# Kernel optimization log

Hardware: AMD Instinct MI355X
Metric: run time of the kernel (lower is better)

The kernel has to match this reference:

```python
import jax, jax.numpy as jnp
import numpy as np

N, E, IN, H, D = 50000, 800000, 256, 4, 32
NEG_SLOPE = 0.2


def setup_inputs() -> dict:
    key = jax.random.key(0)
    ks = jax.random.split(key, 11)
    feat = jax.random.normal(ks[0], (N, IN), jnp.float32)
    src = jax.random.randint(ks[1], (E,), 0, N, jnp.int32)
    dst = jax.random.randint(ks[2], (E,), 0, N, jnp.int32)
    # ppmi in [1, 10) so log(log(ppmi)) path is non-trivial
    ppmi = 1.0 + 9.0 * jax.random.uniform(ks[3], (E,), jnp.float32)
    eps_src = jax.random.normal(ks[4], (N, H, 1), jnp.float32)
    eps_dst = jax.random.normal(ks[5], (N, H, 1), jnp.float32)
    W = jax.random.normal(ks[6], (IN, H * D), jnp.float32) * (1.0 / np.sqrt(IN))
    mu_src = jax.random.normal(ks[7], (1, H, D), jnp.float32) * 0.02
    mu_dst = jax.random.normal(ks[8], (1, H, D), jnp.float32) * 0.02
    lam_src = jax.random.normal(ks[9], (1, H, D), jnp.float32) * 0.02
    lam_dst = jax.random.normal(ks[10], (1, H, D), jnp.float32) * 0.02
    return dict(feat=feat, src=src, dst=dst, ppmi=ppmi, eps_src=eps_src,
                eps_dst=eps_dst, W=W, mu_src=mu_src, mu_dst=mu_dst,
                lam_src=lam_src, lam_dst=lam_dst)


def reference(feat, src, dst, ppmi, eps_src, eps_dst, W, mu_src, mu_dst, lam_src, lam_dst):
    n = feat.shape[0]
    h, d = mu_src.shape[1], mu_src.shape[2]
    ft = (feat @ W).reshape(n, h, d)                      # [N,H,D]
    # per-node attention scalars (src == dst node set here)
    mu_s = (ft * mu_src).sum(-1, keepdims=True)           # [N,H,1]
    lam_s = (ft * lam_src).sum(-1, keepdims=True)
    mu_d = (ft * mu_dst).sum(-1, keepdims=True)
    lam_d = (ft * lam_src).sum(-1, keepdims=True)         # original uses lam_src here (replicated)
    # reparameterize z = eps * exp(0.5*logvar) + mu
    z_src = eps_src * jnp.exp(0.5 * lam_s) + mu_s
    z_dst = eps_dst * jnp.exp(0.5 * lam_d) + mu_d
    e = jax.nn.leaky_relu(z_src[src] + z_dst[dst], NEG_SLOPE)   # [E,H,1]
    scale = jnp.clip(jnp.log(jnp.clip(jnp.log(ppmi), 1.0, None)), 1.0, None)
    e2 = e * scale[:, None, None]
    # edge softmax over destination segments
    emax = jax.ops.segment_max(e2, dst, num_segments=n)   # [N,H,1]
    ee = jnp.exp(e2 - emax[dst])
    denom = jax.ops.segment_sum(ee, dst, num_segments=n)
    a = ee / denom[dst]                                    # [E,H,1]
    # weighted scatter-sum aggregation: u_mul_e + sum
    rst = jax.ops.segment_sum(ft[src] * a, dst, num_segments=n)  # [N,H,D]
    return rst, mu_s + mu_d, lam_s + lam_d
```

## Files before the change

### kernel.cpp

```cpp
#include <hip/hip_runtime.h>

#define N_NODES 50000
#define N_EDGES 800000
#define IN_DIM  256
#define NH      4
#define HD      128
#define NEG_SLOPE 0.2f
#define SCAN_BLOCKS ((N_NODES + 255) / 256)
#define HIST_BLOCKS ((N_EDGES + 255) / 256)
#define WT_BLOCKS   ((HD * IN_DIM) / 256)
#define K1B_BLOCKS  ((N_NODES * NH + 255) / 256)

typedef short          v8s __attribute__((ext_vector_type(8)));
typedef float          v4f __attribute__((ext_vector_type(4)));
typedef float          v2f __attribute__((ext_vector_type(2)));
typedef unsigned short us8 __attribute__((ext_vector_type(8)));
typedef int            v2i __attribute__((ext_vector_type(2)));

__device__ __forceinline__ unsigned short f2bf(float f)
{
    unsigned int u = __float_as_uint(f);
    u += 0x7fffu + ((u >> 16) & 1u);
    return (unsigned short)(u >> 16);
}
__device__ __forceinline__ float bf2f(unsigned int bits16)
{
    return __uint_as_float(bits16 << 16);
}

__device__ __forceinline__ float edge_scale(float p)
{
    const float lp = fmaxf(__logf(p), 1.0f);
    return fmaxf(__logf(lp), 1.0f);
}

__global__ __launch_bounds__(256) void k_wt_hist(
    const float* __restrict__ W, unsigned short* __restrict__ Wt_bf,
    const int* __restrict__ dst, int* __restrict__ counts,
    int* __restrict__ rank)
{
    const int b = blockIdx.x;
    if (b < HIST_BLOCKS) {
        const int e = b * 256 + threadIdx.x;
        if (e < N_EDGES) rank[e] = atomicAdd(&counts[dst[e]], 1);
    } else {
        const int idx = (b - HIST_BLOCKS) * 256 + threadIdx.x;
        const int n = idx >> 8;
        const int k = idx & 255;
        Wt_bf[n * IN_DIM + k] = f2bf(W[(size_t)k * HD + n]);
    }
}

#define AS 40
#define CS 136

__global__ __launch_bounds__(256) void k1_mfma(
    const float* __restrict__ feat, const unsigned short* __restrict__ Wt_bf,
    unsigned short* __restrict__ ft_bf)
{
    __shared__ ushort smem[17408];
    ushort* A_sh = smem;
    ushort* B_sh = smem + 128 * AS;

    const int t    = threadIdx.x;
    const int lane = t & 63;
    const int wv   = t >> 6;
    const int r0   = blockIdx.x * 128;

    const int arow = t >> 3;
    const int akk  = (t & 7) * 4;
    int rA[4];
#pragma unroll
    for (int p = 0; p < 4; ++p) rA[p] = min(r0 + arow + 32 * p, N_NODES - 1);
    const int bn  = t >> 2;
    const int bk8 = (t & 3) * 8;

    float4 fa[4];
    us8    fb[2];

#define LOADC(kc0)                                                              \
    do {                                                                        \
        _Pragma("unroll")                                                       \
        for (int p = 0; p < 4; ++p)                                             \
            fa[p] = *(const float4*)(feat + (size_t)rA[p] * IN_DIM + (kc0) + akk); \
        _Pragma("unroll")                                                       \
        for (int p = 0; p < 2; ++p)                                             \
            fb[p] = *(const us8*)(Wt_bf + (size_t)(bn + 64 * p) * IN_DIM + (kc0) + bk8); \
    } while (0)

    v4f acc[2][8];
#pragma unroll
    for (int i = 0; i < 2; ++i)
#pragma unroll
        for (int j = 0; j < 8; ++j) acc[i][j] = (v4f)(0.0f);

    const int frow = lane & 15;
    const int fq   = lane >> 4;

    LOADC(0);

    for (int c = 0; c < IN_DIM / 32; ++c) {
        __syncthreads();
#pragma unroll
        for (int p = 0; p < 4; ++p) {
            ushort4 u;
            u.x = f2bf(fa[p].x); u.y = f2bf(fa[p].y);
            u.z = f2bf(fa[p].z); u.w = f2bf(fa[p].w);
            *(ushort4*)(A_sh + (arow + 32 * p) * AS + akk) = u;
        }
#pragma unroll
        for (int p = 0; p < 2; ++p)
            *(us8*)(B_sh + (bn + 64 * p) * AS + bk8) = fb[p];
        __syncthreads();

        if (c + 1 < IN_DIM / 32) LOADC((c + 1) * 32);

        v8s a0 = *(const v8s*)(A_sh + (wv * 32 + frow) * AS + fq * 8);
        v8s a1 = *(const v8s*)(A_sh + (wv * 32 + 16 + frow) * AS + fq * 8);
        v8s bfr[8];
#pragma unroll
        for (int nf = 0; nf < 8; ++nf)
            bfr[nf] = *(const v8s*)(B_sh + (nf * 16 + frow) * AS + fq * 8);
#pragma unroll
        for (int nf = 0; nf < 8; ++nf) {
            acc[0][nf] = __builtin_amdgcn_mfma_f32_16x16x32_bf16(
                a0, bfr[nf], acc[0][nf], 0, 0, 0);
            acc[1][nf] = __builtin_amdgcn_mfma_f32_16x16x32_bf16(
                a1, bfr[nf], acc[1][nf], 0, 0, 0);
        }
    }

    __syncthreads();
    ushort* Cw = smem + wv * (32 * CS);
#pragma unroll
    for (int mf = 0; mf < 2; ++mf)
#pragma unroll
        for (int nf = 0; nf < 8; ++nf)
#pragma unroll
            for (int r = 0; r < 4; ++r)
                Cw[(mf * 16 + fq * 4 + r) * CS + nf * 16 + frow] =
                    f2bf(acc[mf][nf][r]);
    __syncthreads();

#pragma unroll
    for (int p = 0; p < 8; ++p) {
        const int row_l = (lane >> 4) + 4 * p;
        const int colv  = (lane & 15) * 8;
        const us8 val = *(const us8*)(Cw + row_l * CS + colv);
        const int grow = r0 + wv * 32 + row_l;
        if (grow < N_NODES)
            *(us8*)(ft_bf + (size_t)grow * HD + colv) = val;
    }
}

__global__ __launch_bounds__(256) void k_k1b_scanlocal(
    const int* __restrict__ counts, int* __restrict__ local,
    int* __restrict__ bsums,
    const unsigned short* __restrict__ ft_bf,
    const float* __restrict__ mu_src, const float* __restrict__ mu_dst,
    const float* __restrict__ lam_src,
    const float* __restrict__ eps_src, const float* __restrict__ eps_dst,
    float* __restrict__ z_src_ws, float* __restrict__ z_dst_ws,
    float* __restrict__ mu_out, float* __restrict__ lam_out)
{
    __shared__ int sh[256];
    const int b = blockIdx.x;
    const int t = threadIdx.x;

    if (b < SCAN_BLOCKS) {
        const int i = b * 256 + t;
        const int v = (i < N_NODES) ? counts[i] : 0;
        sh[t] = v;
        __syncthreads();
#pragma unroll
        for (int off = 1; off < 256; off <<= 1) {
            int x = (t >= off) ? sh[t - off] : 0;
            __syncthreads();
            sh[t] += x;
            __syncthreads();
        }
        if (i < N_NODES) local[i] = sh[t] - v;
        if (t == 255) bsums[b] = sh[255];
        return;
    }

    const int g = (b - SCAN_BLOCKS) * 256 + t;
    if (g >= N_NODES * NH) return;
    const int row = g >> 2;
    const int h   = g & 3;

    const unsigned short* fr = ft_bf + (size_t)row * HD + h * 32;
    const float* ms = mu_src + h * 32;
    const float* md = mu_dst + h * 32;
    const float* ls = lam_src + h * 32;

    float pm = 0.0f, pd = 0.0f, pl = 0.0f;
#pragma unroll
    for (int v = 0; v < 4; ++v) {
        const us8 u = *(const us8*)(fr + v * 8);
#pragma unroll
        for (int j = 0; j < 8; ++j) {
            const float f = bf2f(u[j]);
            const int   i = v * 8 + j;
            pm = fmaf(f, ms[i], pm);
            pd = fmaf(f, md[i], pd);
            pl = fmaf(f, ls[i], pl);
        }
    }
    const float sdev = expf(0.5f * pl);
    z_src_ws[g] = eps_src[g] * sdev + pm;
    z_dst_ws[g] = eps_dst[g] * sdev + pd;
    mu_out[g]   = pm + pd;
    lam_out[g]  = 2.0f * pl;
}

__global__ __launch_bounds__(256) void k_scan_bsums(
    const int* __restrict__ bsums, int* __restrict__ bscan)
{
    __shared__ int sh[256];
    const int t = threadIdx.x;
    const int v = (t < SCAN_BLOCKS) ? bsums[t] : 0;
    sh[t] = v;
    __syncthreads();
#pragma unroll
    for (int off = 1; off < 256; off <<= 1) {
        int x = (t >= off) ? sh[t - off] : 0;
        __syncthreads();
        sh[t] += x;
        __syncthreads();
    }
    if (t < SCAN_BLOCKS) bscan[t] = sh[t] - v;
}

__global__ __launch_bounds__(256) void k_scan_add(
    const int* __restrict__ local, const int* __restrict__ bscan,
    int* __restrict__ offsets)
{
    const int i = blockIdx.x * 256 + threadIdx.x;
    if (i >= N_NODES) return;
    offsets[i] = local[i] + bscan[blockIdx.x];
}

__global__ __launch_bounds__(256) void k_scatter(
    const int* __restrict__ src, const int* __restrict__ dst,
    const float* __restrict__ ppmi, const int* __restrict__ rank,
    const int* __restrict__ offsets, v2i* __restrict__ rec_sorted)
{
    const int e = blockIdx.x * 256 + threadIdx.x;
    if (e >= N_EDGES) return;
    const int d0 = dst[e];
    const int j  = offsets[d0] + rank[e];
    v2i rec;
    rec.x = src[e];
    rec.y = __float_as_int(edge_scale(ppmi[e]));
    __builtin_nontemporal_store(rec, rec_sorted + j);
}

__device__ __forceinline__ float edge_w1(float zs, float zd, float sc)
{
    float v = zs + zd;
    v = (v >= 0.0f) ? v : NEG_SLOPE * v;
    return __expf(v * sc);
}

__global__ __launch_bounds__(256, 8) void k3_csr(
    const int* __restrict__ offsets, const int* __restrict__ counts,
    const v2i* __restrict__ rec_sorted,
    const float* __restrict__ z_src_ws, const float* __restrict__ z_dst_ws,
    const uint4* __restrict__ ft_u128, v2f* __restrict__ rst2)
{
    const int node = blockIdx.x * 4 + (threadIdx.x >> 6);
    const int lane = threadIdx.x & 63;
    const int es   = lane >> 4;
    const int li   = lane & 15;
    const int h    = li >> 2;
    const int start = offsets[node];
    const int deg   = counts[node];
    const float zd  = z_dst_ws[node * NH + h];

    float acc[8] = {0, 0, 0, 0, 0, 0, 0, 0};
    float wsum = 0.0f;

#define K3_EDGE(EI)                                                            \
    do {                                                                       \
        const int  ei  = (EI);                                                 \
        const int  idx = start + ((ei < deg) ? ei : 0);                        \
        const v2i  r   = __builtin_nontemporal_load(rec_sorted + idx);         \
        const float zs = z_src_ws[r.x * NH + h];                               \
        const uint4 f  = ft_u128[(size_t)r.x * 16 + li];                       \
        float w = edge_w1(zs, zd, __int_as_float(r.y));                        \
        if (ei >= deg) w = 0.0f;                                               \
        acc[0] = fmaf(bf2f(f.x & 0xffffu), w, acc[0]);                         \
        acc[1] = fmaf(bf2f(f.x >> 16),     w, acc[1]);                         \
        acc[2] = fmaf(bf2f(f.y & 0xffffu), w, acc[2]);                         \
        acc[3] = fmaf(bf2f(f.y >> 16),     w, acc[3]);                         \
        acc[4] = fmaf(bf2f(f.z & 0xffffu), w, acc[4]);                         \
        acc[5] = fmaf(bf2f(f.z >> 16),     w, acc[5]);                         \
        acc[6] = fmaf(bf2f(f.w & 0xffffu), w, acc[6]);                         \
        acc[7] = fmaf(bf2f(f.w >> 16),     w, acc[7]);                         \
        wsum += w;                                                             \
    } while (0)

    int i = 0;
    for (; i + 16 <= deg; i += 16) {
        K3_EDGE(i + es);
        K3_EDGE(i + 4 + es);
        K3_EDGE(i + 8 + es);
        K3_EDGE(i + 12 + es);
    }
    if (i < deg) {
        K3_EDGE(i + es);
        K3_EDGE(i + 4 + es);
        K3_EDGE(i + 8 + es);
        K3_EDGE(i + 12 + es);
    }

#pragma unroll
    for (int m = 16; m <= 32; m <<= 1) {
        wsum += __shfl_xor(wsum, m, 64);
#pragma unroll
        for (int j = 0; j < 8; ++j) acc[j] += __shfl_xor(acc[j], m, 64);
    }

    const float inv = (wsum > 0.0f) ? 1.0f / wsum : 0.0f;
    v2f o;
    o.x = acc[es * 2] * inv;
    o.y = acc[es * 2 + 1] * inv;
    __builtin_nontemporal_store(o, &rst2[(size_t)node * 64 + li * 4 + es]);
}

extern "C" void kernel_launch(void* const* d_in, const int* in_sizes, int n_in,
                              void* d_out, int out_size, void* d_ws, size_t ws_size,
                              hipStream_t stream)
{
    const float* feat    = (const float*)d_in[0];
    const int*   src     = (const int*)  d_in[1];
    const int*   dst     = (const int*)  d_in[2];
    const float* ppmi    = (const float*)d_in[3];
    const float* eps_src = (const float*)d_in[4];
    const float* eps_dst = (const float*)d_in[5];
    const float* W       = (const float*)d_in[6];
    const float* mu_src  = (const float*)d_in[7];
    const float* mu_dst  = (const float*)d_in[8];
    const float* lam_src = (const float*)d_in[9];

    float* out     = (float*)d_out;
    float* rst     = out;
    float* mu_out  = out + (size_t)N_NODES * HD;
    float* lam_out = mu_out + (size_t)N_NODES * NH;

    char* wsb = (char*)d_ws;
    v2i*            rec_s  = (v2i*)wsb;
    unsigned short* ft_bf  = (unsigned short*)(wsb + (size_t)N_EDGES * 8);
    unsigned short* Wt_bf  = ft_bf + (size_t)N_NODES * HD;
    float*          zs_ws  = (float*)(Wt_bf + (size_t)HD * IN_DIM);
    float*          zd_ws  = zs_ws + (size_t)N_NODES * NH;
    int*            counts = (int*)(zd_ws + (size_t)N_NODES * NH);
    int*            local  = counts + N_NODES;
    int*            offsets= local + N_NODES;
    int*            bsums  = offsets + N_NODES;
    int*            bscan  = bsums + 256;
    int*            rank   = bscan + 256;

    hipMemsetAsync(counts, 0, N_NODES * sizeof(int), stream);

    k_wt_hist<<<HIST_BLOCKS + WT_BLOCKS, 256, 0, stream>>>(
        W, Wt_bf, dst, counts, rank);

    k1_mfma<<<(N_NODES + 127) / 128, 256, 0, stream>>>(feat, Wt_bf, ft_bf);

    k_k1b_scanlocal<<<SCAN_BLOCKS + K1B_BLOCKS, 256, 0, stream>>>(
        counts, local, bsums,
        ft_bf, mu_src, mu_dst, lam_src, eps_src, eps_dst,
        zs_ws, zd_ws, mu_out, lam_out);

    k_scan_bsums<<<1, 256, 0, stream>>>(bsums, bscan);
    k_scan_add<<<SCAN_BLOCKS, 256, 0, stream>>>(local, bscan, offsets);

    k_scatter<<<HIST_BLOCKS, 256, 0, stream>>>(
        src, dst, ppmi, rank, offsets, rec_s);

    k3_csr<<<N_NODES / 4, 256, 0, stream>>>(
        offsets, counts, rec_s, zs_ws, zd_ws,
        (const uint4*)ft_bf, (v2f*)rst);
}
```

Measured before the change: 236.4 us.

## Fuse GEMM epilogue attention scalars and single-pass scan into one kernel

Folds the per-node mu/lam/z computation into the GEMM epilogue, reading the bf16 tile from shared memory instead of reloading ft from global memory. Runs the degree prefix scan as extra blocks of the same launch, with a last-block-done atomic counter doing the block-sum scan. The separate add pass is removed; consumers compute local+bscan on the fly. This cuts three kernel launches and one pass over ft, at the cost of heavier epilogue work and atomic-based cross-block ordering.

```diff
diff --git a/kernel.cpp b/kernel.cpp
--- a/kernel.cpp
+++ b/kernel.cpp
@@ -9,7 +9,7 @@
 #define SCAN_BLOCKS ((N_NODES + 255) / 256)
 #define HIST_BLOCKS ((N_EDGES + 255) / 256)
 #define WT_BLOCKS   ((HD * IN_DIM) / 256)
-#define K1B_BLOCKS  ((N_NODES * NH + 255) / 256)
+#define GEMM_BLOCKS ((N_NODES + 127) / 128)
 
 typedef short          v8s __attribute__((ext_vector_type(8)));
 typedef float          v4f __attribute__((ext_vector_type(4)));
@@ -54,18 +54,70 @@
 #define AS 40
 #define CS 136
 
-__global__ __launch_bounds__(256) void k1_mfma(
+__global__ __launch_bounds__(256) void k_gemm_fused(
     const float* __restrict__ feat, const unsigned short* __restrict__ Wt_bf,
-    unsigned short* __restrict__ ft_bf)
-{
-    __shared__ ushort smem[17408];
+    unsigned short* __restrict__ ft_bf,
+    const int* __restrict__ counts, int* __restrict__ local,
+    int* __restrict__ bsums, int* __restrict__ bscan, int* __restrict__ done,
+    const float* __restrict__ mu_src, const float* __restrict__ mu_dst,
+    const float* __restrict__ lam_src,
+    const float* __restrict__ eps_src, const float* __restrict__ eps_dst,
+    float* __restrict__ z_src_ws, float* __restrict__ z_dst_ws,
+    float* __restrict__ mu_out, float* __restrict__ lam_out)
+{
+    __shared__ ushort smem[17408 + 768];
+    const int t = threadIdx.x;
+    const int b = blockIdx.x;
+
+    if (b >= GEMM_BLOCKS) {
+        int* sh = (int*)smem;
+        __shared__ int lastv;
+        const int sb = b - GEMM_BLOCKS;
+        const int i = sb * 256 + t;
+        const int v = (i < N_NODES) ? counts[i] : 0;
+        sh[t] = v;
+        __syncthreads();
+#pragma unroll
+        for (int off = 1; off < 256; off <<= 1) {
+            int x = (t >= off) ? sh[t - off] : 0;
+            __syncthreads();
+            sh[t] += x;
+            __syncthreads();
+        }
+        if (i < N_NODES) local[i] = sh[t] - v;
+        if (t == 255) atomicExch(&bsums[sb], sh[255]);
+        __syncthreads();
+        if (t == 0) lastv = atomicAdd(done, 1);
+        __syncthreads();
+        if (lastv == SCAN_BLOCKS - 1) {
+            const int v2 = (t < SCAN_BLOCKS) ? atomicAdd(&bsums[t], 0) : 0;
+            sh[t] = v2;
+            __syncthreads();
+#pragma unroll
+            for (int off = 1; off < 256; off <<= 1) {
+                int x = (t >= off) ? sh[t - off] : 0;
+                __syncthreads();
+                sh[t] += x;
+                __syncthreads();
+            }
+            if (t < SCAN_BLOCKS) bscan[t] = sh[t] - v2;
+        }
+        return;
+    }
+
     ushort* A_sh = smem;
     ushort* B_sh = smem + 128 * AS;
-
-    const int t    = threadIdx.x;
+    float*  tab  = (float*)(smem + 17408);
+
+    if (t < 128) {
+        tab[t]       = mu_src[t];
+        tab[128 + t] = mu_dst[t];
+        tab[256 + t] = lam_src[t];
+    }
+
     const int lane = t & 63;
     const int wv   = t >> 6;
-    const int r0   = blockIdx.x * 128;
+    const int r0   = b * 128;
 
     const int arow = t >> 3;
     const int akk  = (t & 7) * 4;
@@ -151,105 +203,48 @@
         if (grow < N_NODES)
             *(us8*)(ft_bf + (size_t)grow * HD + colv) = val;
     }
-}
-
-__global__ __launch_bounds__(256) void k_k1b_scanlocal(
-    const int* __restrict__ counts, int* __restrict__ local,
-    int* __restrict__ bsums,
-    const unsigned short* __restrict__ ft_bf,
-    const float* __restrict__ mu_src, const float* __restrict__ mu_dst,
-    const float* __restrict__ lam_src,
-    const float* __restrict__ eps_src, const float* __restrict__ eps_dst,
-    float* __restrict__ z_src_ws, float* __restrict__ z_dst_ws,
-    float* __restrict__ mu_out, float* __restrict__ lam_out)
-{
-    __shared__ int sh[256];
-    const int b = blockIdx.x;
-    const int t = threadIdx.x;
-
-    if (b < SCAN_BLOCKS) {
-        const int i = b * 256 + t;
-        const int v = (i < N_NODES) ? counts[i] : 0;
-        sh[t] = v;
-        __syncthreads();
-#pragma unroll
-        for (int off = 1; off < 256; off <<= 1) {
-            int x = (t >= off) ? sh[t - off] : 0;
-            __syncthreads();
-            sh[t] += x;
-            __syncthreads();
-        }
-        if (i < N_NODES) local[i] = sh[t] - v;
-        if (t == 255) bsums[b] = sh[255];
-        return;
-    }
-
-    const int g = (b - SCAN_BLOCKS) * 256 + t;
-    if (g >= N_NODES * NH) return;
-    const int row = g >> 2;
-    const int h   = g & 3;
-
-    const unsigned short* fr = ft_bf + (size_t)row * HD + h * 32;
-    const float* ms = mu_src + h * 32;
-    const float* md = mu_dst + h * 32;
-    const float* ls = lam_src + h * 32;
-
-    float pm = 0.0f, pd = 0.0f, pl = 0.0f;
-#pragma unroll
-    for (int v = 0; v < 4; ++v) {
-        const us8 u = *(const us8*)(fr + v * 8);
-#pragma unroll
-        for (int j = 0; j < 8; ++j) {
-            const float f = bf2f(u[j]);
-            const int   i = v * 8 + j;
-            pm = fmaf(f, ms[i], pm);
-            pd = fmaf(f, md[i], pd);
-            pl = fmaf(f, ls[i], pl);
-        }
-    }
-    const float sdev = expf(0.5f * pl);
-    z_src_ws[g] = eps_src[g] * sdev + pm;
-    z_dst_ws[g] = eps_dst[g] * sdev + pd;
-    mu_out[g]   = pm + pd;
-    lam_out[g]  = 2.0f * pl;
-}
-
-__global__ __launch_bounds__(256) void k_scan_bsums(
-    const int* __restrict__ bsums, int* __restrict__ bscan)
-{
-    __shared__ int sh[256];
-    const int t = threadIdx.x;
-    const int v = (t < SCAN_BLOCKS) ? bsums[t] : 0;
-    sh[t] = v;
-    __syncthreads();
-#pragma unroll
-    for (int off = 1; off < 256; off <<= 1) {
-        int x = (t >= off) ? sh[t - off] : 0;
-        __syncthreads();
-        sh[t] += x;
-        __syncthreads();
-    }
-    if (t < SCAN_BLOCKS) bscan[t] = sh[t] - v;
-}
-
-__global__ __launch_bounds__(256) void k_scan_add(
-    const int* __restrict__ local, const int* __restrict__ bscan,
-    int* __restrict__ offsets)
-{
-    const int i = blockIdx.x * 256 + threadIdx.x;
-    if (i >= N_NODES) return;
-    offsets[i] = local[i] + bscan[blockIdx.x];
+
+#pragma unroll
+    for (int tk = 0; tk < 2; ++tk) {
+        const int task = lane + tk * 64;
+        const int row  = task >> 2;
+        const int h    = task & 3;
+        const int grow = r0 + wv * 32 + row;
+        if (grow < N_NODES) {
+            const ushort* cr = Cw + row * CS + h * 32;
+            float pm = 0.0f, pd = 0.0f, pl = 0.0f;
+#pragma unroll
+            for (int v8i = 0; v8i < 4; ++v8i) {
+                const us8 u = *(const us8*)(cr + v8i * 8);
+#pragma unroll
+                for (int j = 0; j < 8; ++j) {
+                    const float f = bf2f(u[j]);
+                    const int   i2 = v8i * 8 + j;
+                    pm = fmaf(f, tab[h * 32 + i2], pm);
+                    pd = fmaf(f, tab[128 + h * 32 + i2], pd);
+                    pl = fmaf(f, tab[256 + h * 32 + i2], pl);
+                }
+            }
+            const int g = grow * NH + h;
+            const float sdev = expf(0.5f * pl);
+            z_src_ws[g] = eps_src[g] * sdev + pm;
+            z_dst_ws[g] = eps_dst[g] * sdev + pd;
+            mu_out[g]   = pm + pd;
+            lam_out[g]  = 2.0f * pl;
+        }
+    }
 }
 
 __global__ __launch_bounds__(256) void k_scatter(
     const int* __restrict__ src, const int* __restrict__ dst,
     const float* __restrict__ ppmi, const int* __restrict__ rank,
-    const int* __restrict__ offsets, v2i* __restrict__ rec_sorted)
+    const int* __restrict__ local, const int* __restrict__ bscan,
+    v2i* __restrict__ rec_sorted)
 {
     const int e = blockIdx.x * 256 + threadIdx.x;
     if (e >= N_EDGES) return;
     const int d0 = dst[e];
-    const int j  = offsets[d0] + rank[e];
+    const int j  = local[d0] + bscan[d0 >> 8] + rank[e];
     v2i rec;
     rec.x = src[e];
     rec.y = __float_as_int(edge_scale(ppmi[e]));
@@ -264,7 +259,8 @@
 }
 
 __global__ __launch_bounds__(256, 8) void k3_csr(
-    const int* __restrict__ offsets, const int* __restrict__ counts,
+    const int* __restrict__ local, const int* __restrict__ bscan,
+    const int* __restrict__ counts,
     const v2i* __restrict__ rec_sorted,
     const float* __restrict__ z_src_ws, const float* __restrict__ z_dst_ws,
     const uint4* __restrict__ ft_u128, v2f* __restrict__ rst2)
@@ -274,7 +270,7 @@
     const int es   = lane >> 4;
     const int li   = lane & 15;
     const int h    = li >> 2;
-    const int start = offsets[node];
+    const int start = local[node] + bscan[node >> 8];
     const int deg   = counts[node];
     const float zd  = z_dst_ws[node * NH + h];
 
@@ -356,31 +352,27 @@
     float*          zs_ws  = (float*)(Wt_bf + (size_t)HD * IN_DIM);
     float*          zd_ws  = zs_ws + (size_t)N_NODES * NH;
     int*            counts = (int*)(zd_ws + (size_t)N_NODES * NH);
-    int*            local  = counts + N_NODES;
-    int*            offsets= local + N_NODES;
-    int*            bsums  = offsets + N_NODES;
+    int*            done   = counts + N_NODES;
+    int*            local  = done + 1;
+    int*            bsums  = local + N_NODES;
     int*            bscan  = bsums + 256;
     int*            rank   = bscan + 256;
 
-    hipMemsetAsync(counts, 0, N_NODES * sizeof(int), stream);
+    hipMemsetAsync(counts, 0, (N_NODES + 1) * sizeof(int), stream);
 
     k_wt_hist<<<HIST_BLOCKS + WT_BLOCKS, 256, 0, stream>>>(
         W, Wt_bf, dst, counts, rank);
 
-    k1_mfma<<<(N_NODES + 127) / 128, 256, 0, stream>>>(feat, Wt_bf, ft_bf);
-
-    k_k1b_scanlocal<<<SCAN_BLOCKS + K1B_BLOCKS, 256, 0, stream>>>(
-        counts, local, bsums,
-        ft_bf, mu_src, mu_dst, lam_src, eps_src, eps_dst,
+    k_gemm_fused<<<GEMM_BLOCKS + SCAN_BLOCKS, 256, 0, stream>>>(
+        feat, Wt_bf, ft_bf,
+        counts, local, bsums, bscan, done,
+        mu_src, mu_dst, lam_src, eps_src, eps_dst,
         zs_ws, zd_ws, mu_out, lam_out);
 
-    k_scan_bsums<<<1, 256, 0, stream>>>(bsums, bscan);
-    k_scan_add<<<SCAN_BLOCKS, 256, 0, stream>>>(local, bscan, offsets);
-
     k_scatter<<<HIST_BLOCKS, 256, 0, stream>>>(
-        src, dst, ppmi, rank, offsets, rec_s);
+        src, dst, ppmi, rank, local, bscan, rec_s);
 
     k3_csr<<<N_NODES / 4, 256, 0, stream>>>(
-        offsets, counts, rec_s, zs_ws, zd_ws,
+        local, bscan, counts, rec_s, zs_ws, zd_ws,
         (const uint4*)ft_bf, (v2f*)rst);
 }
```

Measured after the change: 226.9 us. -4.0%, faster.
